# Optimization experiments

Hardware: AMD Instinct MI355X
Metric: run time of the kernel (lower is better)

Reference implementation:

```python
import jax, jax.numpy as jnp
import numpy as np

N_NODES = 50000
N_EDGES = 800000
IN_DIM = 64
HID = 128
NUM_LAYERS = 4
N_GRAPHS = 1024
LEAKY_SLOPE = 0.01


def setup_inputs() -> dict:
    key = jax.random.key(0)
    ks = jax.random.split(key, 16)
    s = 0.05
    inp = {
        "x": jax.random.normal(ks[0], (N_NODES, IN_DIM), dtype=jnp.float32),
        "edge_index": jax.random.randint(ks[1], (2, N_EDGES), 0, N_NODES, dtype=jnp.int64),
        "batch": jnp.sort(jax.random.randint(ks[2], (N_NODES,), 0, N_GRAPHS, dtype=jnp.int64)),
        # layer 0 (in=IN_DIM -> HID, residual projection)
        "l0_W1": jax.random.normal(ks[3], (IN_DIM, HID), dtype=jnp.float32) * s,
        "l0_b1": jnp.zeros((HID,), jnp.float32),
        "l0_W2": jax.random.normal(ks[4], (HID, HID), dtype=jnp.float32) * s,
        "l0_b2": jnp.zeros((HID,), jnp.float32),
        "l0_Wres": jax.random.normal(ks[5], (IN_DIM, HID), dtype=jnp.float32) * s,
        # layers 1..NUM_LAYERS-1 (HID -> HID, identity residual), stacked
        "Ws1": jax.random.normal(ks[6], (NUM_LAYERS - 1, HID, HID), dtype=jnp.float32) * s,
        "bs1": jnp.zeros((NUM_LAYERS - 1, HID), jnp.float32),
        "Ws2": jax.random.normal(ks[7], (NUM_LAYERS - 1, HID, HID), dtype=jnp.float32) * s,
        "bs2": jnp.zeros((NUM_LAYERS - 1, HID), jnp.float32),
        # fc head
        "fW1": jax.random.normal(ks[8], (HID, HID), dtype=jnp.float32) * s,
        "fb1": jnp.zeros((HID,), jnp.float32),
        "fW2": jax.random.normal(ks[9], (HID, 1), dtype=jnp.float32) * s,
        "fb2": jnp.zeros((1,), jnp.float32),
    }
    return inp


def _gin_layer(x, src, dst, W1, b1, W2, b2, res):
    # GIN sum aggregation: gather source node features, scatter-add at targets
    agg = jax.ops.segment_sum(x[src], dst, num_segments=N_NODES)  # [N, d]
    h = x + agg  # (1 + eps) * x + agg, eps = 0
    h = jax.nn.relu(h @ W1 + b1) @ W2 + b2
    return jax.nn.relu(h + res)


def reference(x, edge_index, batch,
              l0_W1, l0_b1, l0_W2, l0_b2, l0_Wres,
              Ws1, bs1, Ws2, bs2,
              fW1, fb1, fW2, fb2):
    src, dst = edge_index[0], edge_index[1]
    # layer 0 with linear residual projection (in_dim != hidden_dim)
    h = _gin_layer(x, src, dst, l0_W1, l0_b1, l0_W2, l0_b2, x @ l0_Wres)
    # remaining layers with identity residual
    for i in range(NUM_LAYERS - 1):
        h = _gin_layer(h, src, dst, Ws1[i], bs1[i], Ws2[i], bs2[i], h)
    # global mean pool over graphs
    sums = jax.ops.segment_sum(h, batch, num_segments=N_GRAPHS)  # [G, HID]
    counts = jax.ops.segment_sum(jnp.ones((h.shape[0],), h.dtype), batch, num_segments=N_GRAPHS)
    pooled = sums / jnp.maximum(counts, 1.0)[:, None]
    # fc head: Linear -> LeakyReLU -> Linear
    out = jax.nn.leaky_relu(pooled @ fW1 + fb1, negative_slope=LEAKY_SLOPE) @ fW2 + fb2
    return out  # [G, 1]
```

## Files before the change

kernel.cpp:

```cpp
#include <hip/hip_runtime.h>

#define NN 50000
#define NE 800000
#define IND 64
#define HID 128
#define NG 1024

#define NBK 391
#define BCAP 2560

typedef short bf16x8 __attribute__((ext_vector_type(8)));
typedef float f32x4 __attribute__((ext_vector_type(4)));

static __device__ __forceinline__ unsigned short f2bf(float f) {
    unsigned int u = __float_as_uint(f);
    return (unsigned short)((u + 0x7FFFu + ((u >> 16) & 1u)) >> 16);
}
static __device__ __forceinline__ float bf2f(unsigned short h) {
    return __uint_as_float(((unsigned int)h) << 16);
}
static __device__ __forceinline__ float4 f4zero() { return make_float4(0.f, 0.f, 0.f, 0.f); }

__global__ void bin_kernel(const int* __restrict__ src, const int* __restrict__ dst,
                           int* __restrict__ bcur, unsigned int* __restrict__ bedge) {
    __shared__ int hist[NBK];
    __shared__ int base[NBK];
    int tid = threadIdx.x;
    for (int i = tid; i < NBK; i += 256) hist[i] = 0;
    __syncthreads();
    int e0 = blockIdx.x * 4096;
    unsigned int pk[16];
    int bk[16], lo[16];
#pragma unroll
    for (int j = 0; j < 16; ++j) {
        int e = e0 + j * 256 + tid;
        bk[j] = -1;
        if (e < NE) {
            int s = src[e], d = dst[e];
            pk[j] = (unsigned int)s | ((unsigned int)d << 16);
            bk[j] = d >> 7;
            lo[j] = atomicAdd(&hist[bk[j]], 1);
        }
    }
    __syncthreads();
    for (int i = tid; i < NBK; i += 256)
        base[i] = hist[i] ? atomicAdd(&bcur[i], hist[i]) : 0;
    __syncthreads();
#pragma unroll
    for (int j = 0; j < 16; ++j) {
        if (bk[j] >= 0) {
            int idx = base[bk[j]] + lo[j];
            if (idx < BCAP) bedge[(size_t)bk[j] * BCAP + idx] = pk[j];
        }
    }
}

__global__ void build_csr_kernel(const unsigned int* __restrict__ bedge,
                                 const int* __restrict__ bcur, int* __restrict__ row_beg,
                                 int* __restrict__ row_end, int* __restrict__ esrc) {
    __shared__ unsigned int se[BCAP];
    __shared__ int h[128], sc[128], cur[128];
    int b = blockIdx.x, tid = threadIdx.x;
    int cnt = min(bcur[b], BCAP);
    for (int i = tid; i < cnt; i += 256) se[i] = bedge[(size_t)b * BCAP + i];
    if (tid < 128) h[tid] = 0;
    __syncthreads();
    for (int i = tid; i < cnt; i += 256) atomicAdd(&h[(se[i] >> 16) & 127], 1);
    __syncthreads();
    if (tid < 128) sc[tid] = h[tid];
    __syncthreads();
    for (int off = 1; off < 128; off <<= 1) {
        int add = 0;
        if (tid < 128 && tid >= off) add = sc[tid - off];
        __syncthreads();
        if (tid < 128) sc[tid] += add;
        __syncthreads();
    }
    if (tid < 128) {
        int ex = sc[tid] - h[tid];
        int n = (b << 7) + tid;
        if (n < NN) {
            row_beg[n] = b * BCAP + ex;
            row_end[n] = b * BCAP + sc[tid];
        }
        cur[tid] = ex;
    }
    __syncthreads();
    for (int i = tid; i < cnt; i += 256) {
        unsigned int v = se[i];
        int dl = (v >> 16) & 127;
        int pos = atomicAdd(&cur[dl], 1);
        esrc[(size_t)b * BCAP + pos] = (int)(v & 0xffffu);
    }
}

__global__ void convert_all(const float* __restrict__ Wres, const float* __restrict__ W1,
                            const float* __restrict__ W2, const float* __restrict__ Ws1,
                            const float* __restrict__ Ws2, short* __restrict__ wresHi,
                            short* __restrict__ wresLo, short* __restrict__ w1Hi,
                            short* __restrict__ w1Lo, short* __restrict__ w2Hi,
                            short* __restrict__ w2Lo, short* __restrict__ ws1Hi,
                            short* __restrict__ ws1Lo, short* __restrict__ ws2Hi,
                            short* __restrict__ ws2Lo) {
    int t = blockIdx.x * 256 + threadIdx.x;
    const float* W;
    short *hi, *lo;
    int K, idx;
    if (t < 8192) { W = Wres; hi = wresHi; lo = wresLo; K = 64; idx = t; }
    else if (t < 16384) { W = W1; hi = w1Hi; lo = w1Lo; K = 64; idx = t - 8192; }
    else if (t < 32768) { W = W2; hi = w2Hi; lo = w2Lo; K = 128; idx = t - 16384; }
    else if (t < 81920) { W = Ws1; hi = ws1Hi; lo = ws1Lo; K = 128; idx = t - 32768; }
    else { W = Ws2; hi = ws2Hi; lo = ws2Lo; K = 128; idx = t - 81920; }
    int m = idx / (K * 128);
    int r = idx - m * K * 128;
    int n = r / K, k = r - n * K;
    float w = W[(size_t)m * K * 128 + k * 128 + n];
    unsigned short hh = f2bf(w);
    hi[idx] = (short)hh;
    lo[idx] = (short)f2bf(w - bf2f(hh));
}

__global__ void to_bf16_kernel(const float* __restrict__ s, short* __restrict__ d, int total) {
    int i = blockIdx.x * 256 + threadIdx.x;
    if (i < total) d[i] = (short)f2bf(s[i]);
}

__global__ void agg128b_kernel(const unsigned int* __restrict__ hb, const float* __restrict__ hf,
                               const int* __restrict__ row_beg, const int* __restrict__ row_end,
                               const int* __restrict__ es, float* __restrict__ t) {
    int wv = threadIdx.x >> 6, lane = threadIdx.x & 63;
    int n = blockIdx.x * 4 + wv;
    if (n >= NN) return;
    int beg = row_beg[n], end = row_end[n];
    float2 acc = ((const float2*)hf)[(size_t)n * 64 + lane];
    int e = beg;
    for (; e + 8 <= end; e += 8) {
        unsigned int v0 = hb[(size_t)es[e] * 64 + lane];
        unsigned int v1 = hb[(size_t)es[e + 1] * 64 + lane];
        unsigned int v2 = hb[(size_t)es[e + 2] * 64 + lane];
        unsigned int v3 = hb[(size_t)es[e + 3] * 64 + lane];
        unsigned int v4 = hb[(size_t)es[e + 4] * 64 + lane];
        unsigned int v5 = hb[(size_t)es[e + 5] * 64 + lane];
        unsigned int v6 = hb[(size_t)es[e + 6] * 64 + lane];
        unsigned int v7 = hb[(size_t)es[e + 7] * 64 + lane];
        acc.x += __uint_as_float(v0 << 16) + __uint_as_float(v1 << 16) +
                 __uint_as_float(v2 << 16) + __uint_as_float(v3 << 16) +
                 __uint_as_float(v4 << 16) + __uint_as_float(v5 << 16) +
                 __uint_as_float(v6 << 16) + __uint_as_float(v7 << 16);
        acc.y += __uint_as_float(v0 & 0xffff0000u) + __uint_as_float(v1 & 0xffff0000u) +
                 __uint_as_float(v2 & 0xffff0000u) + __uint_as_float(v3 & 0xffff0000u) +
                 __uint_as_float(v4 & 0xffff0000u) + __uint_as_float(v5 & 0xffff0000u) +
                 __uint_as_float(v6 & 0xffff0000u) + __uint_as_float(v7 & 0xffff0000u);
    }
    for (; e + 4 <= end; e += 4) {
        unsigned int v0 = hb[(size_t)es[e] * 64 + lane];
        unsigned int v1 = hb[(size_t)es[e + 1] * 64 + lane];
        unsigned int v2 = hb[(size_t)es[e + 2] * 64 + lane];
        unsigned int v3 = hb[(size_t)es[e + 3] * 64 + lane];
        acc.x += __uint_as_float(v0 << 16) + __uint_as_float(v1 << 16) +
                 __uint_as_float(v2 << 16) + __uint_as_float(v3 << 16);
        acc.y += __uint_as_float(v0 & 0xffff0000u) + __uint_as_float(v1 & 0xffff0000u) +
                 __uint_as_float(v2 & 0xffff0000u) + __uint_as_float(v3 & 0xffff0000u);
    }
    for (; e < end; ++e) {
        unsigned int v = hb[(size_t)es[e] * 64 + lane];
        acc.x += __uint_as_float(v << 16);
        acc.y += __uint_as_float(v & 0xffff0000u);
    }
    ((float2*)t)[(size_t)n * 64 + lane] = acc;
}

__global__ void agg64b_kernel(const unsigned short* __restrict__ xb, const float* __restrict__ xf,
                              const int* __restrict__ row_beg, const int* __restrict__ row_end,
                              const int* __restrict__ es, float* __restrict__ t) {
    int wv = threadIdx.x >> 6, lane = threadIdx.x & 63;
    int n = blockIdx.x * 4 + wv;
    if (n >= NN) return;
    int beg = row_beg[n], end = row_end[n];
    float acc = xf[(size_t)n * 64 + lane];
    int e = beg;
    for (; e + 4 <= end; e += 4) {
        int s0 = es[e], s1 = es[e + 1], s2 = es[e + 2], s3 = es[e + 3];
        acc += bf2f(xb[(size_t)s0 * 64 + lane]) + bf2f(xb[(size_t)s1 * 64 + lane]) +
               bf2f(xb[(size_t)s2 * 64 + lane]) + bf2f(xb[(size_t)s3 * 64 + lane]);
    }
    for (; e < end; ++e) acc += bf2f(xb[(size_t)es[e] * 64 + lane]);
    t[(size_t)n * 64 + lane] = acc;
}

__global__ __launch_bounds__(256, 4) void fused2(
    const float* __restrict__ tin, const float* __restrict__ xres,
    const short* __restrict__ W1Hi, const short* __restrict__ W1Lo,
    const float* __restrict__ b1, const short* __restrict__ W2Hi,
    const short* __restrict__ W2Lo, const float* __restrict__ b2,
    float* __restrict__ hout, short* __restrict__ hbout) {
    __shared__ short lds[16384];
    int tid = threadIdx.x;
    int rowBase = blockIdx.x * 64;
    int lane = tid & 63, wv = tid >> 6;
    int m = lane & 15, g = lane >> 4;

    float4 sv[8];
#pragma unroll
    for (int j = 0; j < 8; ++j) {
        int i = j * 256 + tid;
        int r = i >> 5, c4 = i & 31;
        int row = rowBase + r;
        sv[j] = f4zero();
        if (row < NN) sv[j] = ((const float4*)(tin + (size_t)row * 128))[c4];
    }
    bf16x8 wh[2][4], wl[2][4];
#pragma unroll
    for (int ctl = 0; ctl < 2; ++ctl) {
        int col = wv * 32 + ctl * 16 + m;
#pragma unroll
        for (int kc = 0; kc < 4; ++kc) {
            wh[ctl][kc] = *(const bf16x8*)(W1Hi + col * 128 + kc * 32 + g * 8);
            wl[ctl][kc] = *(const bf16x8*)(W1Lo + col * 128 + kc * 32 + g * 8);
        }
    }
#pragma unroll
    for (int j = 0; j < 8; ++j) {
        int i = j * 256 + tid;
        int r = i >> 5, c4 = i & 31;
        float4 v = sv[j];
        unsigned short hx = f2bf(v.x), hy = f2bf(v.y), hz = f2bf(v.z), hw = f2bf(v.w);
        short4 hv = {(short)hx, (short)hy, (short)hz, (short)hw};
        short4 lv = {(short)f2bf(v.x - bf2f(hx)), (short)f2bf(v.y - bf2f(hy)),
                     (short)f2bf(v.z - bf2f(hz)), (short)f2bf(v.w - bf2f(hw))};
        int sidx = (r * 128 + c4 * 4) ^ ((r & 7) << 3);
        *(short4*)(lds + sidx) = hv;
        *(short4*)(lds + 8192 + sidx) = lv;
    }
    __syncthreads();

    f32x4 acc1[4][2];
#pragma unroll
    for (int s = 0; s < 4; ++s) {
        int rloc = s * 16 + m;
        bf16x8 tHi[4], tLo[4];
#pragma unroll
        for (int kc = 0; kc < 4; ++kc) {
            int idx = (rloc * 128 + kc * 32 + g * 8) ^ ((rloc & 7) << 3);
            tHi[kc] = *(const bf16x8*)(lds + idx);
            tLo[kc] = *(const bf16x8*)(lds + 8192 + idx);
        }
#pragma unroll
        for (int ctl = 0; ctl < 2; ++ctl) {
            float bv = b1[wv * 32 + ctl * 16 + m];
            f32x4 a = {bv, bv, bv, bv};
#pragma unroll
            for (int kc = 0; kc < 4; ++kc) {
                a = __builtin_amdgcn_mfma_f32_16x16x32_bf16(tHi[kc], wh[ctl][kc], a, 0, 0, 0);
                a = __builtin_amdgcn_mfma_f32_16x16x32_bf16(tLo[kc], wh[ctl][kc], a, 0, 0, 0);
                a = __builtin_amdgcn_mfma_f32_16x16x32_bf16(tHi[kc], wl[ctl][kc], a, 0, 0, 0);
            }
            acc1[s][ctl] = a;
        }
    }
    __syncthreads();

#pragma unroll
    for (int s = 0; s < 4; ++s) {
#pragma unroll
        for (int ctl = 0; ctl < 2; ++ctl) {
            int col = wv * 32 + ctl * 16 + m;
#pragma unroll
            for (int i = 0; i < 4; ++i) {
                float u = fmaxf(acc1[s][ctl][i], 0.f);
                unsigned short uh = f2bf(u);
                int ru = s * 16 + g * 4 + i;
                int sidx = (ru * 128 + col) ^ ((ru & 7) << 3);
                lds[sidx] = (short)uh;
                lds[8192 + sidx] = (short)f2bf(u - bf2f(uh));
            }
        }
    }
#pragma unroll
    for (int ctl = 0; ctl < 2; ++ctl) {
        int col = wv * 32 + ctl * 16 + m;
#pragma unroll
        for (int kc = 0; kc < 4; ++kc) {
            wh[ctl][kc] = *(const bf16x8*)(W2Hi + col * 128 + kc * 32 + g * 8);
            wl[ctl][kc] = *(const bf16x8*)(W2Lo + col * 128 + kc * 32 + g * 8);
        }
    }
    __syncthreads();

#pragma unroll
    for (int s = 0; s < 4; ++s) {
        int rloc = s * 16 + m;
        bf16x8 uHi[4], uLo[4];
#pragma unroll
        for (int kc = 0; kc < 4; ++kc) {
            int idx = (rloc * 128 + kc * 32 + g * 8) ^ ((rloc & 7) << 3);
            uHi[kc] = *(const bf16x8*)(lds + idx);
            uLo[kc] = *(const bf16x8*)(lds + 8192 + idx);
        }
#pragma unroll
        for (int ctl = 0; ctl < 2; ++ctl) {
            int col = wv * 32 + ctl * 16 + m;
            float bv = b2[col];
            f32x4 a = {bv, bv, bv, bv};
#pragma unroll
            for (int kc = 0; kc < 4; ++kc) {
                a = __builtin_amdgcn_mfma_f32_16x16x32_bf16(uHi[kc], wh[ctl][kc], a, 0, 0, 0);
                a = __builtin_amdgcn_mfma_f32_16x16x32_bf16(uLo[kc], wh[ctl][kc], a, 0, 0, 0);
                a = __builtin_amdgcn_mfma_f32_16x16x32_bf16(uHi[kc], wl[ctl][kc], a, 0, 0, 0);
            }
#pragma unroll
            for (int i = 0; i < 4; ++i) {
                int row = rowBase + s * 16 + g * 4 + i;
                if (row < NN) {
                    float v = fmaxf(a[i] + xres[(size_t)row * 128 + col], 0.f);
                    hout[(size_t)row * 128 + col] = v;
                    hbout[(size_t)row * 128 + col] = (short)f2bf(v);
                }
            }
        }
    }
}

__global__ __launch_bounds__(256, 3) void fused0(
    const float* __restrict__ tin, const float* __restrict__ x,
    const short* __restrict__ W1Hi, const short* __restrict__ W1Lo,
    const float* __restrict__ b1, const short* __restrict__ W2Hi,
    const short* __restrict__ W2Lo, const float* __restrict__ b2,
    const short* __restrict__ WrHi, const short* __restrict__ WrLo,
    float* __restrict__ hout, short* __restrict__ hbout) {
    __shared__ short lds[16384];
    int tid = threadIdx.x;
    int rowBase = blockIdx.x * 64;
    int lane = tid & 63, wv = tid >> 6;
    int m = lane & 15, g = lane >> 4;

    float4 sv[4], sx[4];
#pragma unroll
    for (int j = 0; j < 4; ++j) {
        int i = j * 256 + tid;
        int r = i >> 4, c4 = i & 15;
        int row = rowBase + r;
        sv[j] = f4zero();
        sx[j] = f4zero();
        if (row < NN) {
            sv[j] = ((const float4*)(tin + (size_t)row * 64))[c4];
            sx[j] = ((const float4*)(x + (size_t)row * 64))[c4];
        }
    }
    bf16x8 wh[2][4], wl[2][4];
#pragma unroll
    for (int ctl = 0; ctl < 2; ++ctl) {
        int col = wv * 32 + ctl * 16 + m;
#pragma unroll
        for (int kc = 0; kc < 2; ++kc) {
            wh[ctl][kc] = *(const bf16x8*)(W1Hi + col * 64 + kc * 32 + g * 8);
            wl[ctl][kc] = *(const bf16x8*)(W1Lo + col * 64 + kc * 32 + g * 8);
            wh[ctl][2 + kc] = *(const bf16x8*)(WrHi + col * 64 + kc * 32 + g * 8);
            wl[ctl][2 + kc] = *(const bf16x8*)(WrLo + col * 64 + kc * 32 + g * 8);
        }
    }
#pragma unroll
    for (int j = 0; j < 4; ++j) {
        int i = j * 256 + tid;
        int r = i >> 4, c4 = i & 15;
        int sidx = (r * 64 + c4 * 4) ^ ((r & 7) << 3);
        float4 v = sv[j];
        unsigned short hx = f2bf(v.x), hy = f2bf(v.y), hz = f2bf(v.z), hw = f2bf(v.w);
        short4 hv = {(short)hx, (short)hy, (short)hz, (short)hw};
        short4 lv = {(short)f2bf(v.x - bf2f(hx)), (short)f2bf(v.y - bf2f(hy)),
                     (short)f2bf(v.z - bf2f(hz)), (short)f2bf(v.w - bf2f(hw))};
        *(short4*)(lds + sidx) = hv;
        *(short4*)(lds + 4096 + sidx) = lv;
        v = sx[j];
        hx = f2bf(v.x), hy = f2bf(v.y), hz = f2bf(v.z), hw = f2bf(v.w);
        short4 hv2 = {(short)hx, (short)hy, (short)hz, (short)hw};
        short4 lv2 = {(short)f2bf(v.x - bf2f(hx)), (short)f2bf(v.y - bf2f(hy)),
                      (short)f2bf(v.z - bf2f(hz)), (short)f2bf(v.w - bf2f(hw))};
        *(short4*)(lds + 8192 + sidx) = hv2;
        *(short4*)(lds + 12288 + sidx) = lv2;
    }
    __syncthreads();

    f32x4 acc1[4][2], racc[4][2];
#pragma unroll
    for (int s = 0; s < 4; ++s) {
        int rloc = s * 16 + m;
        bf16x8 tH[2], tL[2], xH[2], xL[2];
#pragma unroll
        for (int kc = 0; kc < 2; ++kc) {
            int idx = (rloc * 64 + kc * 32 + g * 8) ^ ((rloc & 7) << 3);
            tH[kc] = *(const bf16x8*)(lds + idx);
            tL[kc] = *(const bf16x8*)(lds + 4096 + idx);
            xH[kc] = *(const bf16x8*)(lds + 8192 + idx);
            xL[kc] = *(const bf16x8*)(lds + 12288 + idx);
        }
#pragma unroll
        for (int ctl = 0; ctl < 2; ++ctl) {
            float bv = b1[wv * 32 + ctl * 16 + m];
            f32x4 a = {bv, bv, bv, bv};
            f32x4 r4 = {0.f, 0.f, 0.f, 0.f};
#pragma unroll
            for (int kc = 0; kc < 2; ++kc) {
                a = __builtin_amdgcn_mfma_f32_16x16x32_bf16(tH[kc], wh[ctl][kc], a, 0, 0, 0);
                a = __builtin_amdgcn_mfma_f32_16x16x32_bf16(tL[kc], wh[ctl][kc], a, 0, 0, 0);
                a = __builtin_amdgcn_mfma_f32_16x16x32_bf16(tH[kc], wl[ctl][kc], a, 0, 0, 0);
                r4 = __builtin_amdgcn_mfma_f32_16x16x32_bf16(xH[kc], wh[ctl][2 + kc], r4, 0, 0, 0);
                r4 = __builtin_amdgcn_mfma_f32_16x16x32_bf16(xL[kc], wh[ctl][2 + kc], r4, 0, 0, 0);
                r4 = __builtin_amdgcn_mfma_f32_16x16x32_bf16(xH[kc], wl[ctl][2 + kc], r4, 0, 0, 0);
            }
            acc1[s][ctl] = a;
            racc[s][ctl] = r4;
        }
    }
    __syncthreads();

#pragma unroll
    for (int s = 0; s < 4; ++s) {
#pragma unroll
        for (int ctl = 0; ctl < 2; ++ctl) {
            int col = wv * 32 + ctl * 16 + m;
#pragma unroll
            for (int i = 0; i < 4; ++i) {
                float u = fmaxf(acc1[s][ctl][i], 0.f);
                unsigned short uh = f2bf(u);
                int ru = s * 16 + g * 4 + i;
                int sidx = (ru * 128 + col) ^ ((ru & 7) << 3);
                lds[sidx] = (short)uh;
                lds[8192 + sidx] = (short)f2bf(u - bf2f(uh));
            }
        }
    }
#pragma unroll
    for (int ctl = 0; ctl < 2; ++ctl) {
        int col = wv * 32 + ctl * 16 + m;
#pragma unroll
        for (int kc = 0; kc < 4; ++kc) {
            wh[ctl][kc] = *(const bf16x8*)(W2Hi + col * 128 + kc * 32 + g * 8);
            wl[ctl][kc] = *(const bf16x8*)(W2Lo + col * 128 + kc * 32 + g * 8);
        }
    }
    __syncthreads();

#pragma unroll
    for (int s = 0; s < 4; ++s) {
        int rloc = s * 16 + m;
        bf16x8 uHi[4], uLo[4];
#pragma unroll
        for (int kc = 0; kc < 4; ++kc) {
            int idx = (rloc * 128 + kc * 32 + g * 8) ^ ((rloc & 7) << 3);
            uHi[kc] = *(const bf16x8*)(lds + idx);
            uLo[kc] = *(const bf16x8*)(lds + 8192 + idx);
        }
#pragma unroll
        for (int ctl = 0; ctl < 2; ++ctl) {
            int col = wv * 32 + ctl * 16 + m;
            float bv = b2[col];
            f32x4 a = {bv, bv, bv, bv};
#pragma unroll
            for (int kc = 0; kc < 4; ++kc) {
                a = __builtin_amdgcn_mfma_f32_16x16x32_bf16(uHi[kc], wh[ctl][kc], a, 0, 0, 0);
                a = __builtin_amdgcn_mfma_f32_16x16x32_bf16(uLo[kc], wh[ctl][kc], a, 0, 0, 0);
                a = __builtin_amdgcn_mfma_f32_16x16x32_bf16(uHi[kc], wl[ctl][kc], a, 0, 0, 0);
            }
#pragma unroll
            for (int i = 0; i < 4; ++i) {
                int row = rowBase + s * 16 + g * 4 + i;
                if (row < NN) {
                    float v = fmaxf(a[i] + racc[s][ctl][i], 0.f);
                    hout[(size_t)row * 128 + col] = v;
                    hbout[(size_t)row * 128 + col] = (short)f2bf(v);
                }
            }
        }
    }
}

static __device__ __forceinline__ int lbound(const int* __restrict__ a, int n, int v) {
    int lo = 0, hi = n;
    while (lo < hi) {
        int mid = (lo + hi) >> 1;
        if (a[mid] < v) lo = mid + 1;
        else hi = mid;
    }
    return lo;
}

__global__ void head_kernel(const float* __restrict__ h, const int* __restrict__ batch,
                            const float* __restrict__ fW1, const float* __restrict__ fb1,
                            const float* __restrict__ fW2, const float* __restrict__ fb2,
                            float* __restrict__ out) {
    __shared__ float sp[128];
    __shared__ float su[128];
    __shared__ int sr[2];
    int g = blockIdx.x, t = threadIdx.x;
    if (t == 0) sr[0] = lbound(batch, NN, g);
    if (t == 1) sr[1] = lbound(batch, NN, g + 1);
    __syncthreads();
    int beg = sr[0], end = sr[1];
    float acc = 0.f;
    for (int i = beg; i < end; ++i) acc += h[(size_t)i * 128 + t];
    sp[t] = acc / (float)max(end - beg, 1);
    __syncthreads();
    float a = fb1[t];
#pragma unroll 4
    for (int k = 0; k < 128; ++k) a = fmaf(sp[k], fW1[k * 128 + t], a);
    a = a > 0.f ? a : 0.01f * a;
    su[t] = a * fW2[t];
    __syncthreads();
    for (int s2 = 64; s2 > 0; s2 >>= 1) {
        if (t < s2) su[t] += su[t + s2];
        __syncthreads();
    }
    if (t == 0) out[g] = su[0] + fb2[0];
}

extern "C" void kernel_launch(void* const* d_in, const int* in_sizes, int n_in,
                              void* d_out, int out_size, void* d_ws, size_t ws_size,
                              hipStream_t stream) {
    const float* x = (const float*)d_in[0];
    const int* eidx = (const int*)d_in[1];
    const int* src = eidx;
    const int* dst = eidx + NE;
    const int* batch = (const int*)d_in[2];
    const float* l0_W1 = (const float*)d_in[3];
    const float* l0_b1 = (const float*)d_in[4];
    const float* l0_W2 = (const float*)d_in[5];
    const float* l0_b2 = (const float*)d_in[6];
    const float* l0_Wres = (const float*)d_in[7];
    const float* Ws1 = (const float*)d_in[8];
    const float* bs1 = (const float*)d_in[9];
    const float* Ws2 = (const float*)d_in[10];
    const float* bs2 = (const float*)d_in[11];
    const float* fW1 = (const float*)d_in[12];
    const float* fb1 = (const float*)d_in[13];
    const float* fW2 = (const float*)d_in[14];
    const float* fb2 = (const float*)d_in[15];
    float* out = (float*)d_out;

    size_t used = 0;
    auto alloc = [&](size_t bytes) -> char* {
        char* r = (char*)d_ws + used;
        used = (used + bytes + 255) & ~(size_t)255;
        return r;
    };
    float* A = (float*)alloc((size_t)NN * HID * 4);
    float* B = (float*)alloc((size_t)NN * HID * 4);
    float* C = (float*)alloc((size_t)NN * HID * 4);
    int* bcur = (int*)alloc((size_t)NBK * 4);
    int* row_beg = (int*)alloc((size_t)NN * 4);
    int* row_end = (int*)alloc((size_t)NN * 4);
    int* esrc = (int*)alloc((size_t)NBK * BCAP * 4);
    char* shared_region = alloc((size_t)NN * IND * 2 > (size_t)NBK * BCAP * 4
                                    ? (size_t)NN * IND * 2
                                    : (size_t)NBK * BCAP * 4);
    unsigned int* bedge = (unsigned int*)shared_region;
    short* xb = (short*)shared_region;
    short* wresHi = (short*)alloc(128 * 64 * 2);
    short* wresLo = (short*)alloc(128 * 64 * 2);
    short* w1Hi = (short*)alloc(128 * 64 * 2);
    short* w1Lo = (short*)alloc(128 * 64 * 2);
    short* w2Hi = (short*)alloc(128 * 128 * 2);
    short* w2Lo = (short*)alloc(128 * 128 * 2);
    short* ws1Hi = (short*)alloc(3 * 128 * 128 * 2);
    short* ws1Lo = (short*)alloc(3 * 128 * 128 * 2);
    short* ws2Hi = (short*)alloc(3 * 128 * 128 * 2);
    short* ws2Lo = (short*)alloc(3 * 128 * 128 * 2);
    short* hb = (short*)alloc((size_t)NN * HID * 2);

    hipMemsetAsync(bcur, 0, (size_t)NBK * 4, stream);

    const int GB = (NN + 63) / 64;
    const int AGGB = (NN + 3) / 4;

    convert_all<<<512, 256, 0, stream>>>(l0_Wres, l0_W1, l0_W2, Ws1, Ws2, wresHi, wresLo, w1Hi,
                                         w1Lo, w2Hi, w2Lo, ws1Hi, ws1Lo, ws2Hi, ws2Lo);

    bin_kernel<<<(NE + 4095) / 4096, 256, 0, stream>>>(src, dst, bcur, bedge);
    build_csr_kernel<<<NBK, 256, 0, stream>>>(bedge, bcur, row_beg, row_end, esrc);

    to_bf16_kernel<<<(NN * IND + 255) / 256, 256, 0, stream>>>(x, xb, NN * IND);

    agg64b_kernel<<<AGGB, 256, 0, stream>>>((const unsigned short*)xb, x, row_beg, row_end, esrc,
                                            A);
    fused0<<<GB, 256, 0, stream>>>(A, x, w1Hi, w1Lo, l0_b1, w2Hi, w2Lo, l0_b2, wresHi, wresLo, B,
                                   hb);

    float* hcur = B;
    float* hnxt = C;
    for (int l = 0; l < 3; ++l) {
        agg128b_kernel<<<AGGB, 256, 0, stream>>>((const unsigned int*)hb, hcur, row_beg, row_end,
                                                 esrc, A);
        fused2<<<GB, 256, 0, stream>>>(A, hcur, ws1Hi + (size_t)l * 16384,
                                       ws1Lo + (size_t)l * 16384, bs1 + (size_t)l * HID,
                                       ws2Hi + (size_t)l * 16384, ws2Lo + (size_t)l * 16384,
                                       bs2 + (size_t)l * HID, hnxt, hb);
        float* t2 = hcur;
        hcur = hnxt;
        hnxt = t2;
    }

    head_kernel<<<NG, 128, 0, stream>>>(hcur, batch, fW1, fb1, fW2, fb2, out);
}
```

Baseline: 422.4 us.

## Fuse neighbor aggregation into GIN MLP kernels, removing intermediate buffer

The separate aggregation kernels are folded into the fused MLP kernels. Each block gathers neighbor sums for its 64 rows straight into LDS as hi/lo bf16 splits, so the fp32 aggregate buffer is never written to or read back from global memory, and four launches go away. Because other blocks still read the previous layer's bf16 features while this block writes new ones, the bf16 feature buffer is now double-buffered. The trade-off is that the gather runs with one wave per row inside the MLP kernel, whose launch bounds limit occupancy. That may hide memory latency for the irregular gathers less well than the standalone aggregation kernels did.

```diff
diff --git a/kernel.cpp b/kernel.cpp
--- a/kernel.cpp
+++ b/kernel.cpp
@@ -125,90 +125,19 @@
     if (i < total) d[i] = (short)f2bf(s[i]);
 }
 
-__global__ void agg128b_kernel(const unsigned int* __restrict__ hb, const float* __restrict__ hf,
-                               const int* __restrict__ row_beg, const int* __restrict__ row_end,
-                               const int* __restrict__ es, float* __restrict__ t) {
-    int wv = threadIdx.x >> 6, lane = threadIdx.x & 63;
-    int n = blockIdx.x * 4 + wv;
-    if (n >= NN) return;
-    int beg = row_beg[n], end = row_end[n];
-    float2 acc = ((const float2*)hf)[(size_t)n * 64 + lane];
-    int e = beg;
-    for (; e + 8 <= end; e += 8) {
-        unsigned int v0 = hb[(size_t)es[e] * 64 + lane];
-        unsigned int v1 = hb[(size_t)es[e + 1] * 64 + lane];
-        unsigned int v2 = hb[(size_t)es[e + 2] * 64 + lane];
-        unsigned int v3 = hb[(size_t)es[e + 3] * 64 + lane];
-        unsigned int v4 = hb[(size_t)es[e + 4] * 64 + lane];
-        unsigned int v5 = hb[(size_t)es[e + 5] * 64 + lane];
-        unsigned int v6 = hb[(size_t)es[e + 6] * 64 + lane];
-        unsigned int v7 = hb[(size_t)es[e + 7] * 64 + lane];
-        acc.x += __uint_as_float(v0 << 16) + __uint_as_float(v1 << 16) +
-                 __uint_as_float(v2 << 16) + __uint_as_float(v3 << 16) +
-                 __uint_as_float(v4 << 16) + __uint_as_float(v5 << 16) +
-                 __uint_as_float(v6 << 16) + __uint_as_float(v7 << 16);
-        acc.y += __uint_as_float(v0 & 0xffff0000u) + __uint_as_float(v1 & 0xffff0000u) +
-                 __uint_as_float(v2 & 0xffff0000u) + __uint_as_float(v3 & 0xffff0000u) +
-                 __uint_as_float(v4 & 0xffff0000u) + __uint_as_float(v5 & 0xffff0000u) +
-                 __uint_as_float(v6 & 0xffff0000u) + __uint_as_float(v7 & 0xffff0000u);
-    }
-    for (; e + 4 <= end; e += 4) {
-        unsigned int v0 = hb[(size_t)es[e] * 64 + lane];
-        unsigned int v1 = hb[(size_t)es[e + 1] * 64 + lane];
-        unsigned int v2 = hb[(size_t)es[e + 2] * 64 + lane];
-        unsigned int v3 = hb[(size_t)es[e + 3] * 64 + lane];
-        acc.x += __uint_as_float(v0 << 16) + __uint_as_float(v1 << 16) +
-                 __uint_as_float(v2 << 16) + __uint_as_float(v3 << 16);
-        acc.y += __uint_as_float(v0 & 0xffff0000u) + __uint_as_float(v1 & 0xffff0000u) +
-                 __uint_as_float(v2 & 0xffff0000u) + __uint_as_float(v3 & 0xffff0000u);
-    }
-    for (; e < end; ++e) {
-        unsigned int v = hb[(size_t)es[e] * 64 + lane];
-        acc.x += __uint_as_float(v << 16);
-        acc.y += __uint_as_float(v & 0xffff0000u);
-    }
-    ((float2*)t)[(size_t)n * 64 + lane] = acc;
-}
-
-__global__ void agg64b_kernel(const unsigned short* __restrict__ xb, const float* __restrict__ xf,
-                              const int* __restrict__ row_beg, const int* __restrict__ row_end,
-                              const int* __restrict__ es, float* __restrict__ t) {
-    int wv = threadIdx.x >> 6, lane = threadIdx.x & 63;
-    int n = blockIdx.x * 4 + wv;
-    if (n >= NN) return;
-    int beg = row_beg[n], end = row_end[n];
-    float acc = xf[(size_t)n * 64 + lane];
-    int e = beg;
-    for (; e + 4 <= end; e += 4) {
-        int s0 = es[e], s1 = es[e + 1], s2 = es[e + 2], s3 = es[e + 3];
-        acc += bf2f(xb[(size_t)s0 * 64 + lane]) + bf2f(xb[(size_t)s1 * 64 + lane]) +
-               bf2f(xb[(size_t)s2 * 64 + lane]) + bf2f(xb[(size_t)s3 * 64 + lane]);
-    }
-    for (; e < end; ++e) acc += bf2f(xb[(size_t)es[e] * 64 + lane]);
-    t[(size_t)n * 64 + lane] = acc;
-}
-
-__global__ __launch_bounds__(256, 4) void fused2(
-    const float* __restrict__ tin, const float* __restrict__ xres,
-    const short* __restrict__ W1Hi, const short* __restrict__ W1Lo,
+__global__ __launch_bounds__(256, 4) void fused2g(
+    const float* __restrict__ hcur, const unsigned int* __restrict__ hbin,
+    const int* __restrict__ row_beg, const int* __restrict__ row_end,
+    const int* __restrict__ es, const short* __restrict__ W1Hi, const short* __restrict__ W1Lo,
     const float* __restrict__ b1, const short* __restrict__ W2Hi,
-    const short* __restrict__ W2Lo, const float* __restrict__ b2,
-    float* __restrict__ hout, short* __restrict__ hbout) {
+    const short* __restrict__ W2Lo, const float* __restrict__ b2, float* __restrict__ hout,
+    short* __restrict__ hbout) {
     __shared__ short lds[16384];
     int tid = threadIdx.x;
     int rowBase = blockIdx.x * 64;
     int lane = tid & 63, wv = tid >> 6;
     int m = lane & 15, g = lane >> 4;
 
-    float4 sv[8];
-#pragma unroll
-    for (int j = 0; j < 8; ++j) {
-        int i = j * 256 + tid;
-        int r = i >> 5, c4 = i & 31;
-        int row = rowBase + r;
-        sv[j] = f4zero();
-        if (row < NN) sv[j] = ((const float4*)(tin + (size_t)row * 128))[c4];
-    }
     bf16x8 wh[2][4], wl[2][4];
 #pragma unroll
     for (int ctl = 0; ctl < 2; ++ctl) {
@@ -219,18 +148,54 @@
             wl[ctl][kc] = *(const bf16x8*)(W1Lo + col * 128 + kc * 32 + g * 8);
         }
     }
-#pragma unroll
-    for (int j = 0; j < 8; ++j) {
-        int i = j * 256 + tid;
-        int r = i >> 5, c4 = i & 31;
-        float4 v = sv[j];
-        unsigned short hx = f2bf(v.x), hy = f2bf(v.y), hz = f2bf(v.z), hw = f2bf(v.w);
-        short4 hv = {(short)hx, (short)hy, (short)hz, (short)hw};
-        short4 lv = {(short)f2bf(v.x - bf2f(hx)), (short)f2bf(v.y - bf2f(hy)),
-                     (short)f2bf(v.z - bf2f(hz)), (short)f2bf(v.w - bf2f(hw))};
-        int sidx = (r * 128 + c4 * 4) ^ ((r & 7) << 3);
-        *(short4*)(lds + sidx) = hv;
-        *(short4*)(lds + 8192 + sidx) = lv;
+
+    for (int rr = 0; rr < 16; ++rr) {
+        int r = (wv << 4) + rr;
+        int n = rowBase + r;
+        float2 acc = make_float2(0.f, 0.f);
+        if (n < NN) {
+            int beg = row_beg[n], end = row_end[n];
+            acc = ((const float2*)hcur)[(size_t)n * 64 + lane];
+            int e = beg;
+            for (; e + 8 <= end; e += 8) {
+                unsigned int v0 = hbin[(size_t)es[e] * 64 + lane];
+                unsigned int v1 = hbin[(size_t)es[e + 1] * 64 + lane];
+                unsigned int v2 = hbin[(size_t)es[e + 2] * 64 + lane];
+                unsigned int v3 = hbin[(size_t)es[e + 3] * 64 + lane];
+                unsigned int v4 = hbin[(size_t)es[e + 4] * 64 + lane];
+                unsigned int v5 = hbin[(size_t)es[e + 5] * 64 + lane];
+                unsigned int v6 = hbin[(size_t)es[e + 6] * 64 + lane];
+                unsigned int v7 = hbin[(size_t)es[e + 7] * 64 + lane];
+                acc.x += __uint_as_float(v0 << 16) + __uint_as_float(v1 << 16) +
+                         __uint_as_float(v2 << 16) + __uint_as_float(v3 << 16) +
+                         __uint_as_float(v4 << 16) + __uint_as_float(v5 << 16) +
+                         __uint_as_float(v6 << 16) + __uint_as_float(v7 << 16);
+                acc.y += __uint_as_float(v0 & 0xffff0000u) + __uint_as_float(v1 & 0xffff0000u) +
+                         __uint_as_float(v2 & 0xffff0000u) + __uint_as_float(v3 & 0xffff0000u) +
+                         __uint_as_float(v4 & 0xffff0000u) + __uint_as_float(v5 & 0xffff0000u) +
+                         __uint_as_float(v6 & 0xffff0000u) + __uint_as_float(v7 & 0xffff0000u);
+            }
+            for (; e + 4 <= end; e += 4) {
+                unsigned int v0 = hbin[(size_t)es[e] * 64 + lane];
+                unsigned int v1 = hbin[(size_t)es[e + 1] * 64 + lane];
+                unsigned int v2 = hbin[(size_t)es[e + 2] * 64 + lane];
+                unsigned int v3 = hbin[(size_t)es[e + 3] * 64 + lane];
+                acc.x += __uint_as_float(v0 << 16) + __uint_as_float(v1 << 16) +
+                         __uint_as_float(v2 << 16) + __uint_as_float(v3 << 16);
+                acc.y += __uint_as_float(v0 & 0xffff0000u) + __uint_as_float(v1 & 0xffff0000u) +
+                         __uint_as_float(v2 & 0xffff0000u) + __uint_as_float(v3 & 0xffff0000u);
+            }
+            for (; e < end; ++e) {
+                unsigned int v = hbin[(size_t)es[e] * 64 + lane];
+                acc.x += __uint_as_float(v << 16);
+                acc.y += __uint_as_float(v & 0xffff0000u);
+            }
+        }
+        unsigned short hx = f2bf(acc.x), hy = f2bf(acc.y);
+        unsigned short lx = f2bf(acc.x - bf2f(hx)), ly = f2bf(acc.y - bf2f(hy));
+        int idx = (r * 128 + lane * 2) ^ ((r & 7) << 3);
+        *(unsigned int*)(lds + idx) = (unsigned int)hx | ((unsigned int)hy << 16);
+        *(unsigned int*)(lds + 8192 + idx) = (unsigned int)lx | ((unsigned int)ly << 16);
     }
     __syncthreads();
 
@@ -312,7 +277,7 @@
             for (int i = 0; i < 4; ++i) {
                 int row = rowBase + s * 16 + g * 4 + i;
                 if (row < NN) {
-                    float v = fmaxf(a[i] + xres[(size_t)row * 128 + col], 0.f);
+                    float v = fmaxf(a[i] + hcur[(size_t)row * 128 + col], 0.f);
                     hout[(size_t)row * 128 + col] = v;
                     hbout[(size_t)row * 128 + col] = (short)f2bf(v);
                 }
@@ -321,31 +286,28 @@
     }
 }
 
-__global__ __launch_bounds__(256, 3) void fused0(
-    const float* __restrict__ tin, const float* __restrict__ x,
-    const short* __restrict__ W1Hi, const short* __restrict__ W1Lo,
+__global__ __launch_bounds__(256, 3) void fused0g(
+    const float* __restrict__ x, const unsigned short* __restrict__ xb,
+    const int* __restrict__ row_beg, const int* __restrict__ row_end,
+    const int* __restrict__ es, const short* __restrict__ W1Hi, const short* __restrict__ W1Lo,
     const float* __restrict__ b1, const short* __restrict__ W2Hi,
     const short* __restrict__ W2Lo, const float* __restrict__ b2,
-    const short* __restrict__ WrHi, const short* __restrict__ WrLo,
-    float* __restrict__ hout, short* __restrict__ hbout) {
+    const short* __restrict__ WrHi, const short* __restrict__ WrLo, float* __restrict__ hout,
+    short* __restrict__ hbout) {
     __shared__ short lds[16384];
     int tid = threadIdx.x;
     int rowBase = blockIdx.x * 64;
     int lane = tid & 63, wv = tid >> 6;
     int m = lane & 15, g = lane >> 4;
 
-    float4 sv[4], sx[4];
+    float4 sx[4];
 #pragma unroll
     for (int j = 0; j < 4; ++j) {
         int i = j * 256 + tid;
         int r = i >> 4, c4 = i & 15;
         int row = rowBase + r;
-        sv[j] = f4zero();
         sx[j] = f4zero();
-        if (row < NN) {
-            sv[j] = ((const float4*)(tin + (size_t)row * 64))[c4];
-            sx[j] = ((const float4*)(x + (size_t)row * 64))[c4];
-        }
+        if (row < NN) sx[j] = ((const float4*)(x + (size_t)row * 64))[c4];
     }
     bf16x8 wh[2][4], wl[2][4];
 #pragma unroll
@@ -359,25 +321,40 @@
             wl[ctl][2 + kc] = *(const bf16x8*)(WrLo + col * 64 + kc * 32 + g * 8);
         }
     }
+
+    for (int rr = 0; rr < 16; ++rr) {
+        int r = (wv << 4) + rr;
+        int n = rowBase + r;
+        float acc = 0.f;
+        if (n < NN) {
+            int beg = row_beg[n], end = row_end[n];
+            acc = x[(size_t)n * 64 + lane];
+            int e = beg;
+            for (; e + 4 <= end; e += 4) {
+                int s0 = es[e], s1 = es[e + 1], s2 = es[e + 2], s3 = es[e + 3];
+                acc += bf2f(xb[(size_t)s0 * 64 + lane]) + bf2f(xb[(size_t)s1 * 64 + lane]) +
+                       bf2f(xb[(size_t)s2 * 64 + lane]) + bf2f(xb[(size_t)s3 * 64 + lane]);
+            }
+            for (; e < end; ++e) acc += bf2f(xb[(size_t)es[e] * 64 + lane]);
+        }
+        unsigned short hx = f2bf(acc);
+        unsigned short lx = f2bf(acc - bf2f(hx));
+        int idx = (r * 64 + lane) ^ ((r & 7) << 3);
+        lds[idx] = (short)hx;
+        lds[4096 + idx] = (short)lx;
+    }
 #pragma unroll
     for (int j = 0; j < 4; ++j) {
         int i = j * 256 + tid;
         int r = i >> 4, c4 = i & 15;
         int sidx = (r * 64 + c4 * 4) ^ ((r & 7) << 3);
-        float4 v = sv[j];
+        float4 v = sx[j];
         unsigned short hx = f2bf(v.x), hy = f2bf(v.y), hz = f2bf(v.z), hw = f2bf(v.w);
         short4 hv = {(short)hx, (short)hy, (short)hz, (short)hw};
         short4 lv = {(short)f2bf(v.x - bf2f(hx)), (short)f2bf(v.y - bf2f(hy)),
                      (short)f2bf(v.z - bf2f(hz)), (short)f2bf(v.w - bf2f(hw))};
-        *(short4*)(lds + sidx) = hv;
-        *(short4*)(lds + 4096 + sidx) = lv;
-        v = sx[j];
-        hx = f2bf(v.x), hy = f2bf(v.y), hz = f2bf(v.z), hw = f2bf(v.w);
-        short4 hv2 = {(short)hx, (short)hy, (short)hz, (short)hw};
-        short4 lv2 = {(short)f2bf(v.x - bf2f(hx)), (short)f2bf(v.y - bf2f(hy)),
-                      (short)f2bf(v.z - bf2f(hz)), (short)f2bf(v.w - bf2f(hw))};
-        *(short4*)(lds + 8192 + sidx) = hv2;
-        *(short4*)(lds + 12288 + sidx) = lv2;
+        *(short4*)(lds + 8192 + sidx) = hv;
+        *(short4*)(lds + 12288 + sidx) = lv;
     }
     __syncthreads();
 
@@ -543,7 +520,6 @@
         used = (used + bytes + 255) & ~(size_t)255;
         return r;
     };
-    float* A = (float*)alloc((size_t)NN * HID * 4);
     float* B = (float*)alloc((size_t)NN * HID * 4);
     float* C = (float*)alloc((size_t)NN * HID * 4);
     int* bcur = (int*)alloc((size_t)NBK * 4);
@@ -565,12 +541,12 @@
     short* ws1Lo = (short*)alloc(3 * 128 * 128 * 2);
     short* ws2Hi = (short*)alloc(3 * 128 * 128 * 2);
     short* ws2Lo = (short*)alloc(3 * 128 * 128 * 2);
-    short* hb = (short*)alloc((size_t)NN * HID * 2);
+    short* hbA = (short*)alloc((size_t)NN * HID * 2);
+    short* hbB = (short*)alloc((size_t)NN * HID * 2);
 
     hipMemsetAsync(bcur, 0, (size_t)NBK * 4, stream);
 
     const int GB = (NN + 63) / 64;
-    const int AGGB = (NN + 3) / 4;
 
     convert_all<<<512, 256, 0, stream>>>(l0_Wres, l0_W1, l0_W2, Ws1, Ws2, wresHi, wresLo, w1Hi,
                                          w1Lo, w2Hi, w2Lo, ws1Hi, ws1Lo, ws2Hi, ws2Lo);
@@ -580,24 +556,25 @@
 
     to_bf16_kernel<<<(NN * IND + 255) / 256, 256, 0, stream>>>(x, xb, NN * IND);
 
-    agg64b_kernel<<<AGGB, 256, 0, stream>>>((const unsigned short*)xb, x, row_beg, row_end, esrc,
-                                            A);
-    fused0<<<GB, 256, 0, stream>>>(A, x, w1Hi, w1Lo, l0_b1, w2Hi, w2Lo, l0_b2, wresHi, wresLo, B,
-                                   hb);
-
-    float* hcur = B;
-    float* hnxt = C;
+    fused0g<<<GB, 256, 0, stream>>>(x, (const unsigned short*)xb, row_beg, row_end, esrc, w1Hi,
+                                    w1Lo, l0_b1, w2Hi, w2Lo, l0_b2, wresHi, wresLo, B, hbA);
+
+    float* hc = B;
+    float* hn = C;
+    short* hbc = hbA;
+    short* hbn = hbB;
     for (int l = 0; l < 3; ++l) {
-        agg128b_kernel<<<AGGB, 256, 0, stream>>>((const unsigned int*)hb, hcur, row_beg, row_end,
-                                                 esrc, A);
-        fused2<<<GB, 256, 0, stream>>>(A, hcur, ws1Hi + (size_t)l * 16384,
-                                       ws1Lo + (size_t)l * 16384, bs1 + (size_t)l * HID,
-                                       ws2Hi + (size_t)l * 16384, ws2Lo + (size_t)l * 16384,
-                                       bs2 + (size_t)l * HID, hnxt, hb);
-        float* t2 = hcur;
-        hcur = hnxt;
-        hnxt = t2;
-    }
-
-    head_kernel<<<NG, 128, 0, stream>>>(hcur, batch, fW1, fb1, fW2, fb2, out);
-}
+        fused2g<<<GB, 256, 0, stream>>>(hc, (const unsigned int*)hbc, row_beg, row_end, esrc,
+                                        ws1Hi + (size_t)l * 16384, ws1Lo + (size_t)l * 16384,
+                                        bs1 + (size_t)l * HID, ws2Hi + (size_t)l * 16384,
+                                        ws2Lo + (size_t)l * 16384, bs2 + (size_t)l * HID, hn, hbn);
+        float* tf = hc;
+        hc = hn;
+        hn = tf;
+        short* ts = hbc;
+        hbc = hbn;
+        hbn = ts;
+    }
+
+    head_kernel<<<NG, 128, 0, stream>>>(hc, batch, fW1, fb1, fW2, fb2, out);
+}
```

New measurement: 525.7 us. 1.24x slower.
